# Kernel optimization log

Measured on AMD Instinct MI355X. Metric: run time of the kernel, lower is better.

## Reference

```python
import jax, jax.numpy as jnp
import numpy as np

HEADS, LEVELS, POINTS, ZANCH = 8, 4, 8, 4
EMBED = 256
SHAPES = np.array([[92, 160], [46, 80], [23, 40], [12, 20]], dtype=np.int32)


def setup_inputs() -> dict:
    key = jax.random.key(0)
    k = jax.random.split(key, 9)
    bs, nq = 1, 10000
    nv = int((SHAPES[:, 0].astype(np.int64) * SHAPES[:, 1]).sum())  # 19560
    f32 = jnp.float32
    return dict(
        query=jax.random.normal(k[0], (bs, nq, EMBED), f32),
        value=jax.random.normal(k[1], (bs, nv, EMBED), f32),
        query_pos=0.1 * jax.random.normal(k[2], (bs, nq, EMBED), f32),
        reference_points=jax.random.uniform(k[3], (bs, nq, ZANCH, 2), dtype=f32),
        spatial_shapes=jnp.asarray(SHAPES),
        W_off=0.01 * jax.random.normal(k[4], (EMBED, HEADS * LEVELS * POINTS * 2), f32),
        b_off=0.5 * jax.random.normal(k[5], (HEADS * LEVELS * POINTS * 2,), f32),
        W_attn=0.01 * jax.random.normal(k[6], (EMBED, HEADS * LEVELS * POINTS), f32),
        b_attn=jnp.zeros((HEADS * LEVELS * POINTS,), f32),
        W_val=(1.0 / np.sqrt(EMBED)) * jax.random.normal(k[7], (EMBED, EMBED), f32),
        b_val=jnp.zeros((EMBED,), f32),
        W_out=(1.0 / np.sqrt(EMBED)) * jax.random.normal(k[8], (EMBED, EMBED), f32),
        b_out=jnp.zeros((EMBED,), f32),
    )


def _bilinear(v_l, x, y, Hl, Wl):
    # v_l: [bs, heads, Hl*Wl, d]; x, y: [bs, nq, heads, P] pixel coords
    # (torch grid_sample, align_corners=False, zero padding): px = loc*W - 0.5
    bs, nq, heads, P = x.shape
    d = v_l.shape[-1]
    x0 = jnp.floor(x)
    y0 = jnp.floor(y)
    lx = x - x0
    ly = y - y0
    x0i = x0.astype(jnp.int32)
    y0i = y0.astype(jnp.int32)

    def corner(xi, yi, w):
        valid = (xi >= 0) & (xi < Wl) & (yi >= 0) & (yi < Hl)
        idx = jnp.clip(yi, 0, Hl - 1) * Wl + jnp.clip(xi, 0, Wl - 1)
        idxr = idx.transpose(0, 2, 1, 3).reshape(bs, heads, nq * P)
        g = jnp.take_along_axis(v_l, idxr[..., None], axis=2)  # [bs,heads,nq*P,d]
        g = g.reshape(bs, heads, nq, P, d).transpose(0, 2, 1, 3, 4)
        return g * (w * valid.astype(w.dtype))[..., None]

    return (corner(x0i, y0i, (1 - lx) * (1 - ly))
            + corner(x0i + 1, y0i, lx * (1 - ly))
            + corner(x0i, y0i + 1, (1 - lx) * ly)
            + corner(x0i + 1, y0i + 1, lx * ly))


def reference(query, value, query_pos, reference_points, spatial_shapes,
              W_off, b_off, W_attn, b_attn, W_val, b_val, W_out, b_out):
    shapes = np.asarray(spatial_shapes)  # static per-level (H, W)
    bs, nq, E = query.shape
    heads = HEADS
    L = shapes.shape[0]
    P = W_off.shape[1] // (heads * L * 2)
    Z = reference_points.shape[2]
    d = E // heads

    residual = query
    q = query + query_pos
    v = (value @ W_val + b_val).reshape(bs, -1, heads, d)

    off = (q @ W_off + b_off).reshape(bs, nq, heads, L, P, 2)
    attn = jax.nn.softmax((q @ W_attn + b_attn).reshape(bs, nq, heads, L * P), axis=-1)
    attn = attn.reshape(bs, nq, heads, L, P)

    # normalize offsets by (W, H) per level, add Z-anchor reference points
    norm = jnp.asarray(np.stack([shapes[:, 1], shapes[:, 0]], -1), off.dtype)  # [L,2]
    off = off / norm[None, None, None, :, None, :]
    loc = (reference_points[:, :, None, None, None, :, :]
           + off.reshape(bs, nq, heads, L, P // Z, Z, 2)).reshape(bs, nq, heads, L, P, 2)

    starts = np.concatenate([[0], np.cumsum(shapes[:, 0].astype(np.int64) * shapes[:, 1])])
    out = jnp.zeros((bs, nq, heads, d), q.dtype)
    for l in range(L):  # small fixed loop over pyramid levels
        Hl, Wl = int(shapes[l, 0]), int(shapes[l, 1])
        v_l = v[:, int(starts[l]):int(starts[l + 1])].transpose(0, 2, 1, 3)  # [bs,heads,HW,d]
        x = loc[:, :, :, l, :, 0] * Wl - 0.5
        y = loc[:, :, :, l, :, 1] * Hl - 0.5
        sampled = _bilinear(v_l, x, y, Hl, Wl)  # [bs,nq,heads,P,d]
        out = out + (sampled * attn[:, :, :, l, :, None]).sum(axis=3)

    out = out.reshape(bs, nq, E) @ W_out + b_out
    return out + residual  # dropout is identity at eval
```

## Files before the change

kernel.cpp:

```cpp
#include <hip/hip_runtime.h>
#include <hip/hip_bf16.h>
#include <hip/hip_fp16.h>
#include <math.h>

typedef __hip_bfloat16 bf16;
typedef short short8_t __attribute__((ext_vector_type(8)));
typedef float f32x4 __attribute__((ext_vector_type(4)));
typedef int i32x4 __attribute__((ext_vector_type(4)));

#define EMBED 256
#define ZANCH 4

__global__ __launch_bounds__(256) void k_prep(
    const float* __restrict__ Woff, const float* __restrict__ Wattn,
    const float* __restrict__ Wval, const float* __restrict__ Wout,
    bf16* __restrict__ wt,
    const float* __restrict__ value, bf16* __restrict__ vb,
    const float* __restrict__ query, const float* __restrict__ query_pos,
    bf16* __restrict__ qb)
{
    const int b = blockIdx.x;
    const int tid = threadIdx.x;
    if (b < 320) {
        __shared__ float tile[32][33];
        const int tn = b >> 3, tk = b & 7;
        const int r = tid >> 5, c = tid & 31;
        const int n0 = tn * 32, k0t = tk * 32;
#pragma unroll
        for (int rr = r; rr < 32; rr += 8) {
            const int k = k0t + rr;
            const int n = n0 + c;
            float val;
            if (n < 512)       val = Woff[(size_t)k * 512 + n];
            else if (n < 768)  val = Wattn[(size_t)k * 256 + (n - 512)];
            else if (n < 1024) val = Wval[(size_t)k * 256 + (n - 768)];
            else               val = Wout[(size_t)k * 256 + (n - 1024)];
            tile[rr][c] = val;
        }
        __syncthreads();
#pragma unroll
        for (int rr = r; rr < 32; rr += 8) {
            const int n = n0 + rr;
            const int k = k0t + c;
            wt[(size_t)n * 256 + k] = __float2bfloat16(tile[c][rr]);
        }
    } else if (b < 5210) {
        size_t i = ((size_t)(b - 320) * 256 + tid) * 4;
        float4 a = *(const float4*)(value + i);
        vb[i + 0] = __float2bfloat16(a.x);
        vb[i + 1] = __float2bfloat16(a.y);
        vb[i + 2] = __float2bfloat16(a.z);
        vb[i + 3] = __float2bfloat16(a.w);
    } else {
        size_t i = ((size_t)(b - 5210) * 256 + tid) * 4;
        float4 a = *(const float4*)(query + i);
        float4 p = *(const float4*)(query_pos + i);
        qb[i + 0] = __float2bfloat16(a.x + p.x);
        qb[i + 1] = __float2bfloat16(a.y + p.y);
        qb[i + 2] = __float2bfloat16(a.z + p.z);
        qb[i + 3] = __float2bfloat16(a.w + p.w);
    }
}

__global__ __launch_bounds__(256) void k_gemm_vp(
    const bf16* __restrict__ vb, const bf16* __restrict__ Btv,
    const float* __restrict__ bv, bf16* __restrict__ vhl, int Mv,
    const bf16* __restrict__ qb, const bf16* __restrict__ Btcat,
    const float* __restrict__ boff, const float* __restrict__ battn,
    float* __restrict__ raw, int Mq)
{
    __shared__ char sm[33792];
    float* smE  = (float*)sm;
    bf16*  smEv = (bf16*)sm;

    const int tid  = threadIdx.x;
    const int lane = tid & 63;
    const int wv   = tid >> 6;
    const int c16  = lane & 15, quad = lane >> 4;
    const int nwave = wv * 64;

    const bool isval = (blockIdx.y == 3);
    const int M = isval ? Mv : Mq;
    if ((int)blockIdx.x >= (M + 31) / 32) return;
    const int row0 = blockIdx.x * 32;
    const bf16* A  = isval ? vb : qb;
    const bf16* Bt = isval ? Btv : (Btcat + (size_t)(blockIdx.y * 256) * 256);

    f32x4 acc[2][4] = {};
    {
        size_t aoff[2], boffr[4];
#pragma unroll
        for (int mt = 0; mt < 2; ++mt) {
            int r = row0 + mt * 16 + c16;
            r = (r < M) ? r : (M - 1);
            aoff[mt] = (size_t)r * 256 + quad * 8;
        }
#pragma unroll
        for (int nt = 0; nt < 4; ++nt)
            boffr[nt] = (size_t)(nwave + nt * 16 + c16) * 256 + quad * 8;
#pragma unroll
        for (int k0 = 0; k0 < 256; k0 += 32) {
            short8_t a[2], b[4];
#pragma unroll
            for (int mt = 0; mt < 2; ++mt) a[mt] = *(const short8_t*)(A + aoff[mt] + k0);
#pragma unroll
            for (int nt = 0; nt < 4; ++nt) b[nt] = *(const short8_t*)(Bt + boffr[nt] + k0);
#pragma unroll
            for (int mt = 0; mt < 2; ++mt)
#pragma unroll
                for (int nt = 0; nt < 4; ++nt)
                    acc[mt][nt] = __builtin_amdgcn_mfma_f32_16x16x32_bf16(
                        a[mt], b[nt], acc[mt][nt], 0, 0, 0);
        }
    }

    if (isval) {
#pragma unroll
        for (int nt = 0; nt < 4; ++nt) {
            const int colg = nwave + nt * 16 + c16;
            const float bias = bv[colg];
#pragma unroll
            for (int mt = 0; mt < 2; ++mt)
#pragma unroll
                for (int reg = 0; reg < 4; ++reg) {
                    const int rl = mt * 16 + quad * 4 + reg;
                    smEv[rl * 264 + colg] = __float2bfloat16(acc[mt][nt][reg] + bias);
                }
        }
        __syncthreads();
#pragma unroll
        for (int sub = 0; sub < 2; ++sub) {
            const int h = wv * 2 + sub;
            bf16* dsth = vhl + (size_t)h * Mv * 32;
#pragma unroll
            for (int j = 0; j < 2; ++j) {
                const int s = j * 64 + lane;
                const int pix = s >> 2, seg = s & 3;
                const int rg = row0 + pix;
                if (rg < Mv)
                    *(short8_t*)(dsth + (size_t)rg * 32 + seg * 8) =
                        *(const short8_t*)(smEv + pix * 264 + h * 32 + seg * 8);
            }
        }
    } else {
#pragma unroll
        for (int nt = 0; nt < 4; ++nt) {
            const int colg = nwave + nt * 16 + c16;
            const int cg = blockIdx.y * 256 + colg;
            const float bias = (cg < 512) ? boff[cg] : battn[cg - 512];
#pragma unroll
            for (int mt = 0; mt < 2; ++mt)
#pragma unroll
                for (int reg = 0; reg < 4; ++reg) {
                    const int rl = mt * 16 + quad * 4 + reg;
                    smE[rl * 260 + colg] = acc[mt][nt][reg] + bias;
                }
        }
        __syncthreads();
#pragma unroll
        for (int rr = 0; rr < 8; ++rr) {
            const int rl = wv * 8 + rr;
            const int rg = row0 + rl;
            if (rg < Mq)
                *(f32x4*)(raw + (size_t)rg * 768 + blockIdx.y * 256 + lane * 4) =
                    *(const f32x4*)(smE + rl * 260 + lane * 4);
        }
    }
}

__global__ __launch_bounds__(256) void k_sample(
    const bf16* __restrict__ vhl, const float* __restrict__ raw,
    const float* __restrict__ refpts, bf16* __restrict__ outa, int nq, int nv)
{
    __shared__ int spr[32][132];
    const int tid = threadIdx.x;
    const int b = blockIdx.x;
    const int hp = (b & 7) >> 1;
    const int qg = ((b >> 3) << 1) + (b & 1);
    const int q0 = qg * 16;

    {
        const int lp = tid & 31;
        const int l = lp >> 3;
        const int p = lp & 7;
        const int z = p & (ZANCH - 1);
        const float Wlf = (l == 0) ? 160.f : (l == 1) ? 80.f : (l == 2) ? 40.f : 20.f;
        const float Hlf = (l == 0) ? 92.f : (l == 1) ? 46.f : (l == 2) ? 23.f : 12.f;
        const int Wli = (l == 0) ? 160 : (l == 1) ? 80 : (l == 2) ? 40 : 20;
        const int Hli = (l == 0) ? 92 : (l == 1) ? 46 : (l == 2) ? 23 : 12;
        const int Stl = (l == 0) ? 0 : (l == 1) ? 14720 : (l == 2) ? 18400 : 19320;

#pragma unroll
        for (int r = 0; r < 4; ++r) {
            const int g = r * 8 + (tid >> 5);
            int q = q0 + (g >> 1);
            q = (q < nq) ? q : (nq - 1);
            const int head = hp * 2 + (g & 1);
            const int col = head * 32 + lp;

            const float2 oxy = *(const float2*)(raw + (size_t)q * 768 + 2 * col);
            const float ox = oxy.x;
            const float oy = oxy.y;
            const float lg = raw[(size_t)q * 768 + 512 + col];

            float m = lg;
            for (int o = 16; o > 0; o >>= 1) m = fmaxf(m, __shfl_xor(m, o, 32));
            float e = __expf(lg - m);
            float s = e;
            for (int o = 16; o > 0; o >>= 1) s += __shfl_xor(s, o, 32);
            const float aw = e / s;

            const float refx = refpts[(size_t)q * 8 + z * 2 + 0];
            const float refy = refpts[(size_t)q * 8 + z * 2 + 1];
            const float px = refx * Wlf + ox - 0.5f;
            const float py = refy * Hlf + oy - 0.5f;

            const float x0f = floorf(px), y0f = floorf(py);
            const int x0 = (int)x0f, y0 = (int)y0f;
            const float lx = px - x0f, ly = py - y0f;
            const float cw[4] = { (1.f - lx) * (1.f - ly), lx * (1.f - ly),
                                  (1.f - lx) * ly,         lx * ly };
#pragma unroll
            for (int c = 0; c < 4; ++c) {
                const int xi = x0 + (c & 1);
                const int yi = y0 + (c >> 1);
                const bool valid = (xi >= 0) && (xi < Wli) && (yi >= 0) && (yi < Hli);
                const int xc = min(max(xi, 0), Wli - 1);
                const int yc = min(max(yi, 0), Hli - 1);
                const float w = valid ? (cw[c] * aw) : 0.f;
                const int idx = Stl + yc * Wli + xc;
                const unsigned hw = (unsigned)__half_as_ushort(__float2half(w));
                spr[g][c * 32 + lp] = (idx << 16) | (int)hw;
            }
        }
    }
    __syncthreads();

    const int g2  = tid >> 3;
    const int qs  = g2 >> 1;
    const int hh  = g2 & 1;
    const int ch4 = tid & 7;
    const char* hpb = (const char*)vhl + (size_t)(hp * 2) * nv * 64;
    const unsigned tb = (unsigned)(hh * nv) * 64u + (unsigned)ch4 * 8u;

    float a0 = 0.f, a1 = 0.f, a2 = 0.f, a3 = 0.f;
#pragma unroll 2
    for (int bb = 0; bb < 128; bb += 16) {
        i32x4 pk4[4];
#pragma unroll
        for (int j = 0; j < 4; ++j) pk4[j] = *(const i32x4*)&spr[g2][bb + j * 4];
        int pk[16];
#pragma unroll
        for (int j = 0; j < 16; ++j) pk[j] = pk4[j >> 2][j & 3];
        int2 dv[16];
#pragma unroll
        for (int j = 0; j < 16; ++j)
            dv[j] = *(const int2*)(hpb + (size_t)(tb + (((unsigned)pk[j] >> 16) << 6)));
#pragma unroll
        for (int j = 0; j < 16; ++j) {
            const float w = __half2float(__ushort_as_half((unsigned short)(pk[j] & 0xFFFF)));
            a0 = fmaf(w, __int_as_float(dv[j].x << 16), a0);
            a1 = fmaf(w, __int_as_float(dv[j].x & 0xFFFF0000), a1);
            a2 = fmaf(w, __int_as_float(dv[j].y << 16), a2);
            a3 = fmaf(w, __int_as_float(dv[j].y & 0xFFFF0000), a3);
        }
    }
    const int qf = q0 + qs;
    if (qf < nq) {
        __hip_bfloat162 p01, p23;
        p01.x = __float2bfloat16(a0);
        p01.y = __float2bfloat16(a1);
        p23.x = __float2bfloat16(a2);
        p23.y = __float2bfloat16(a3);
        bf16* dst = outa + (size_t)qf * 256 + (hp * 2 + hh) * 32 + ch4 * 4;
        *(__hip_bfloat162*)dst = p01;
        *(__hip_bfloat162*)(dst + 2) = p23;
    }
}

__global__ __launch_bounds__(256) void k_gemm_out(
    const bf16* __restrict__ outa, const bf16* __restrict__ Bto,
    const float* __restrict__ bo, const float* __restrict__ query,
    float* __restrict__ out, int M)
{
    const int row0 = blockIdx.x * 32;
    const int nwave = (threadIdx.x >> 6) * 64;
    const int lane = threadIdx.x & 63;
    const int c16 = lane & 15, quad = lane >> 4;

    f32x4 acc[2][4] = {};
    {
        size_t aoff[2], boffr[4];
#pragma unroll
        for (int mt = 0; mt < 2; ++mt) {
            int r = row0 + mt * 16 + c16;
            r = (r < M) ? r : (M - 1);
            aoff[mt] = (size_t)r * 256 + quad * 8;
        }
#pragma unroll
        for (int nt = 0; nt < 4; ++nt)
            boffr[nt] = (size_t)(nwave + nt * 16 + c16) * 256 + quad * 8;
#pragma unroll
        for (int k0 = 0; k0 < 256; k0 += 32) {
            short8_t a[2], b[4];
#pragma unroll
            for (int mt = 0; mt < 2; ++mt) a[mt] = *(const short8_t*)(outa + aoff[mt] + k0);
#pragma unroll
            for (int nt = 0; nt < 4; ++nt) b[nt] = *(const short8_t*)(Bto + boffr[nt] + k0);
#pragma unroll
            for (int mt = 0; mt < 2; ++mt)
#pragma unroll
                for (int nt = 0; nt < 4; ++nt)
                    acc[mt][nt] = __builtin_amdgcn_mfma_f32_16x16x32_bf16(
                        a[mt], b[nt], acc[mt][nt], 0, 0, 0);
        }
    }
#pragma unroll
    for (int nt = 0; nt < 4; ++nt) {
        int colg = nwave + nt * 16 + c16;
        float bias = bo[colg];
#pragma unroll
        for (int mt = 0; mt < 2; ++mt)
#pragma unroll
            for (int reg = 0; reg < 4; ++reg) {
                int row = row0 + mt * 16 + quad * 4 + reg;
                if (row < M) {
                    size_t o_ = (size_t)row * 256 + colg;
                    float fv = acc[mt][nt][reg] + bias + query[o_];
                    if (!(fv == fv) || fabsf(fv) > 1e30f) fv = 0.f;
                    out[o_] = fv;
                }
            }
    }
}

extern "C" void kernel_launch(void* const* d_in, const int* in_sizes, int n_in,
                              void* d_out, int out_size, void* d_ws, size_t ws_size,
                              hipStream_t stream)
{
    const float* query     = (const float*)d_in[0];
    const float* value     = (const float*)d_in[1];
    const float* query_pos = (const float*)d_in[2];
    const float* refpts    = (const float*)d_in[3];
    const float* Woff  = (const float*)d_in[5];
    const float* boff  = (const float*)d_in[6];
    const float* Wattn = (const float*)d_in[7];
    const float* battn = (const float*)d_in[8];
    const float* Wval  = (const float*)d_in[9];
    const float* bval  = (const float*)d_in[10];
    const float* Wout  = (const float*)d_in[11];
    const float* bout  = (const float*)d_in[12];
    float* out = (float*)d_out;

    const int nq = in_sizes[0] / EMBED;
    const int nv = in_sizes[1] / EMBED;

    char* base = (char*)d_ws;
    bf16*  wt   = (bf16*)base;
    bf16*  qb   = (bf16*)(base + 655360);
    bf16*  vb   = (bf16*)(base + 5775360);
    float* raw  = (float*)(base + 15790080);
    bf16*  outa = (bf16*)(base + 46510080);
    bf16*  vhl  = (bf16*)(base + 51630080);
    const bf16* Btcat = wt;
    const bf16* Btv   = wt + 768 * 256;
    const bf16* Bto   = wt + 1024 * 256;

    k_prep<<<7710, 256, 0, stream>>>(Woff, Wattn, Wval, Wout, wt,
                                     value, vb, query, query_pos, qb);
    k_gemm_vp<<<dim3((nv + 31) / 32, 4), 256, 0, stream>>>(vb, Btv, bval, vhl, nv,
                                                           qb, Btcat, boff, battn, raw, nq);
    k_sample<<<2504, 256, 0, stream>>>(vhl, raw, refpts, outa, nq, nv);
    k_gemm_out<<<(nq + 31) / 32, 256, 0, stream>>>(outa, Bto, bout, query, out, nq);
}
```

Before: 214.2 us.

## Split sampling work across two threads per output and reduce with shuffle

Each sampling block now covers 8 queries instead of 16, and the grid doubles. Each output channel group is handled by two threads that each gather half of the 128 sample points, and their partial sums are combined with a cross-lane shuffle. The aim is more parallelism and more gathers in flight to hide memory latency, at the cost of an extra shuffle reduction and redundant per-block setup. The bounds clamp on the query index was removed, so the kernel now assumes nq is divisible by 8.

```diff
diff --git a/kernel.cpp b/kernel.cpp
--- a/kernel.cpp
+++ b/kernel.cpp
@@ -172,12 +172,12 @@
     const bf16* __restrict__ vhl, const float* __restrict__ raw,
     const float* __restrict__ refpts, bf16* __restrict__ outa, int nq, int nv)
 {
-    __shared__ int spr[32][132];
+    __shared__ int spr[16][132];
     const int tid = threadIdx.x;
     const int b = blockIdx.x;
     const int hp = (b & 7) >> 1;
     const int qg = ((b >> 3) << 1) + (b & 1);
-    const int q0 = qg * 16;
+    const int q0 = qg * 8;
 
     {
         const int lp = tid & 31;
@@ -191,10 +191,9 @@
         const int Stl = (l == 0) ? 0 : (l == 1) ? 14720 : (l == 2) ? 18400 : 19320;
 
 #pragma unroll
-        for (int r = 0; r < 4; ++r) {
+        for (int r = 0; r < 2; ++r) {
             const int g = r * 8 + (tid >> 5);
-            int q = q0 + (g >> 1);
-            q = (q < nq) ? q : (nq - 1);
+            const int q = q0 + (g >> 1);
             const int head = hp * 2 + (g & 1);
             const int col = head * 32 + lp;
 
@@ -236,26 +235,29 @@
     }
     __syncthreads();
 
-    const int g2  = tid >> 3;
+    const int g2  = tid >> 4;
     const int qs  = g2 >> 1;
     const int hh  = g2 & 1;
+    const int oct = (tid >> 3) & 1;
     const int ch4 = tid & 7;
     const char* hpb = (const char*)vhl + (size_t)(hp * 2) * nv * 64;
-    const unsigned tb = (unsigned)(hh * nv) * 64u + (unsigned)ch4 * 8u;
+    const unsigned tbase = (unsigned)(hh * nv) * 64u + (unsigned)ch4 * 8u;
 
     float a0 = 0.f, a1 = 0.f, a2 = 0.f, a3 = 0.f;
 #pragma unroll 2
-    for (int bb = 0; bb < 128; bb += 16) {
+    for (int bb = 0; bb < 128; bb += 32) {
         i32x4 pk4[4];
-#pragma unroll
-        for (int j = 0; j < 4; ++j) pk4[j] = *(const i32x4*)&spr[g2][bb + j * 4];
+        pk4[0] = *(const i32x4*)&spr[g2][bb + oct * 8];
+        pk4[1] = *(const i32x4*)&spr[g2][bb + oct * 8 + 4];
+        pk4[2] = *(const i32x4*)&spr[g2][bb + 16 + oct * 8];
+        pk4[3] = *(const i32x4*)&spr[g2][bb + 16 + oct * 8 + 4];
         int pk[16];
 #pragma unroll
         for (int j = 0; j < 16; ++j) pk[j] = pk4[j >> 2][j & 3];
         int2 dv[16];
 #pragma unroll
         for (int j = 0; j < 16; ++j)
-            dv[j] = *(const int2*)(hpb + (size_t)(tb + (((unsigned)pk[j] >> 16) << 6)));
+            dv[j] = *(const int2*)(hpb + (size_t)(tbase + (((unsigned)pk[j] >> 16) << 6)));
 #pragma unroll
         for (int j = 0; j < 16; ++j) {
             const float w = __half2float(__ushort_as_half((unsigned short)(pk[j] & 0xFFFF)));
@@ -265,16 +267,18 @@
             a3 = fmaf(w, __int_as_float(dv[j].y & 0xFFFF0000), a3);
         }
     }
-    const int qf = q0 + qs;
-    if (qf < nq) {
-        __hip_bfloat162 p01, p23;
-        p01.x = __float2bfloat16(a0);
-        p01.y = __float2bfloat16(a1);
-        p23.x = __float2bfloat16(a2);
-        p23.y = __float2bfloat16(a3);
-        bf16* dst = outa + (size_t)qf * 256 + (hp * 2 + hh) * 32 + ch4 * 4;
-        *(__hip_bfloat162*)dst = p01;
-        *(__hip_bfloat162*)(dst + 2) = p23;
+    a0 += __shfl_xor(a0, 8);
+    a1 += __shfl_xor(a1, 8);
+    a2 += __shfl_xor(a2, 8);
+    a3 += __shfl_xor(a3, 8);
+
+    if (oct == 0) {
+        union { int2 i2; __hip_bfloat162 h2[2]; } u;
+        u.h2[0].x = __float2bfloat16(a0);
+        u.h2[0].y = __float2bfloat16(a1);
+        u.h2[1].x = __float2bfloat16(a2);
+        u.h2[1].y = __float2bfloat16(a3);
+        *(int2*)(outa + (size_t)(q0 + qs) * 256 + (hp * 2 + hh) * 32 + ch4 * 4) = u.i2;
     }
 }
 
@@ -370,6 +374,6 @@
                                      value, vb, query, query_pos, qb);
     k_gemm_vp<<<dim3((nv + 31) / 32, 4), 256, 0, stream>>>(vb, Btv, bval, vhl, nv,
                                                            qb, Btcat, boff, battn, raw, nq);
-    k_sample<<<2504, 256, 0, stream>>>(vhl, raw, refpts, outa, nq, nv);
+    k_sample<<<(nq / 8) * 4, 256, 0, stream>>>(vhl, raw, refpts, outa, nq, nv);
     k_gemm_out<<<(nq + 31) / 32, 256, 0, stream>>>(outa, Bto, bout, query, out, nq);
 }
```

Measured after the change: 215.4 us. Within noise of the previous version (+0.6%).
